# Performance work log

Hardware: AMD Instinct MI355X
Metric: run time of the kernel (lower is better)

## Reference

```python
import jax, jax.numpy as jnp
import numpy as np

THRESH1 = 0.8      # snn.Leaky threshold
THRESH2 = 1.0      # snn.Synaptic default threshold
FS_SLOPE = 25.0    # surrogate.fast_sigmoid default slope
ATAN_ALPHA = 2.0   # surrogate.atan default alpha
TIME_STEPS = 20

# --- surrogate-gradient spike fns (forward = Heaviside) ---
@jax.custom_vjp
def spike_fs(x):
    return (x > 0).astype(x.dtype)
def _fs_fwd(x):
    return (x > 0).astype(x.dtype), x
def _fs_bwd(res, g):
    return (g / (FS_SLOPE * jnp.abs(res) + 1.0) ** 2,)
spike_fs.defvjp(_fs_fwd, _fs_bwd)

@jax.custom_vjp
def spike_atan(x):
    return (x > 0).astype(x.dtype)
def _at_fwd(x):
    return (x > 0).astype(x.dtype), x
def _at_bwd(res, g):
    return (g * (ATAN_ALPHA / 2.0) / (1.0 + (jnp.pi / 2.0 * ATAN_ALPHA * res) ** 2),)
spike_atan.defvjp(_at_fwd, _at_bwd)


def setup_inputs() -> dict:
    key = jax.random.key(0)
    ks = jax.random.split(key, 4)
    V, E, H, B, S = 32000, 256, 512, 8, 16
    x = jax.random.randint(ks[0], (B, S), 0, V)
    embed = jax.random.normal(ks[1], (V, E), jnp.float32)
    W1 = jax.random.normal(ks[2], (H, E), jnp.float32) / jnp.sqrt(jnp.float32(E))
    b1 = jnp.zeros((H,), jnp.float32)
    W2 = jax.random.normal(ks[3], (V, H), jnp.float32) / jnp.sqrt(jnp.float32(H))
    b2 = jnp.zeros((V,), jnp.float32)
    return dict(x=x, embed=embed, W1=W1, b1=b1, W2=W2, b2=b2,
                beta1=jnp.float32(0.85), alpha2=jnp.float32(0.9), beta2=jnp.float32(0.8))


def _forward(x, embed, W1, b1, W2, b2, beta1, alpha2, beta2):
    B, S = x.shape
    V, H = W2.shape
    b1c = jnp.clip(beta1, 0.0, 1.0)   # snntorch clamps learnable decays
    a2c = jnp.clip(alpha2, 0.0, 1.0)
    b2c = jnp.clip(beta2, 0.0, 1.0)
    # cur1 = fc1(embed(x[:, t])) is constant within the inner time loop
    cur1_all = jnp.einsum('bse,he->bsh', embed[x], W1) + b1  # (B, S, H)

    def seq_step(carry, cur1_t):              # cur1_t: (B, H)
        mem1, syn2, mem2 = carry

        def time_step(c, _):
            mem1, syn2, mem2, _ = c
            # Leaky: reset (subtract) from PREVIOUS mem, detached
            reset1 = jax.lax.stop_gradient((mem1 - THRESH1 > 0).astype(mem1.dtype))
            mem1 = b1c * mem1 + cur1_t - reset1 * THRESH1
            spk1 = spike_fs(mem1 - THRESH1)
            cur2 = spk1 @ W2.T + b2            # (B, V)
            # Synaptic: syn = a*syn + cur; mem = b*mem + syn - reset*thr
            reset2 = jax.lax.stop_gradient((mem2 - THRESH2 > 0).astype(mem2.dtype))
            syn2 = a2c * syn2 + cur2
            mem2 = b2c * mem2 + syn2 - reset2 * THRESH2
            spk2 = spike_atan(mem2 - THRESH2)
            return (mem1, syn2, mem2, spk2), None

        spk2_init = jnp.zeros_like(mem2)
        (mem1, syn2, mem2, spk2), _ = jax.lax.scan(
            time_step, (mem1, syn2, mem2, spk2_init), None, length=TIME_STEPS)
        return (mem1, syn2, mem2), spk2       # only last inner spk2 is emitted

    mem1 = jnp.zeros((B, H), jnp.float32)
    syn2 = jnp.zeros((B, V), jnp.float32)
    mem2 = jnp.zeros((B, V), jnp.float32)
    (mem1, syn2, mem2), outs = jax.lax.scan(
        seq_step, (mem1, syn2, mem2), jnp.swapaxes(cur1_all, 0, 1))
    return jnp.swapaxes(outs, 0, 1), mem1, syn2, mem2   # (B, S, V), states


def reference(x, embed, W1, b1, W2, b2, beta1, alpha2, beta2):
    return _forward(x, embed, W1, b1, W2, b2, beta1, alpha2, beta2)
```

## Files before the change

### kernel.cpp

```cpp
#include <hip/hip_runtime.h>
#include <cstdint>

constexpr int NV = 32000;
constexpr int NE = 256;
constexpr int NH = 512;
constexpr int NB = 8;
constexpr int NS = 16;
constexpr int NT = 20;
constexpr float TH1 = 0.8f;
constexpr float TH2 = 1.0f;

typedef _Float16 f16x8 __attribute__((ext_vector_type(8)));
typedef float f32x4 __attribute__((ext_vector_type(4)));

__device__ inline float clip01(float v) { return fminf(fmaxf(v, 0.f), 1.f); }

#define GL_LDS(gp, lp) \
  __builtin_amdgcn_global_load_lds((const __attribute__((address_space(1))) void*)(gp), \
                                   (__attribute__((address_space(3))) void*)(lp), 16, 0, 0)

__device__ inline void barsched() {
  __builtin_amdgcn_s_barrier();
  __builtin_amdgcn_sched_barrier(0);
}

__global__ __launch_bounds__(64) void k_front(
    const int* __restrict__ x, const float* __restrict__ embed,
    const float* __restrict__ W1, const float* __restrict__ b1,
    const float* __restrict__ pbeta1,
    _Float16* __restrict__ A2P, float* __restrict__ mem1_out) {
  __shared__ float emb[16][256];
  const int tid = threadIdx.x;
  const int b   = blockIdx.x >> 3;
  const int hg  = blockIdx.x & 7;
  const int h   = hg * 64 + tid;

  for (int i = tid; i < 16 * 256; i += 64) {
    const int s = i >> 8;
    const int e = i & 255;
    emb[s][e] = embed[(size_t)x[b * 16 + s] * NE + e];
  }
  __syncthreads();

  float c[16];
#pragma unroll
  for (int s = 0; s < 16; ++s) c[s] = 0.f;
  const float* w = W1 + (size_t)h * NE;
  for (int e4 = 0; e4 < 64; ++e4) {
    const float4 wv = *(const float4*)(w + e4 * 4);
#pragma unroll
    for (int s = 0; s < 16; ++s) {
      const float4 ev = *(const float4*)&emb[s][e4 * 4];
      c[s] = fmaf(wv.w, ev.w, fmaf(wv.z, ev.z, fmaf(wv.y, ev.y, fmaf(wv.x, ev.x, c[s]))));
    }
  }
  const float bias = b1[h];
#pragma unroll
  for (int s = 0; s < 16; ++s) c[s] = c[s] + bias;

  const float bc = clip01(pbeta1[0]);
  const _Float16 one  = (_Float16)1.0f;
  const _Float16 zero = (_Float16)0.0f;
  const int ks  = hg;
  const int col = tid ^ (b << 3);
  float mem = 0.f;
  for (int s = 0; s < NS; ++s) {
    const float cs = c[s];
    for (int t = 0; t < NT; ++t) {
      float rst = (mem > TH1) ? TH1 : 0.f;
      mem = __fsub_rn(__fadd_rn(__fmul_rn(bc, mem), cs), rst);
      bool spk = mem > TH1;
      int gs = s * NT + t;
      size_t addr = ((size_t)((gs >> 3) * 8 + ks)) * 4096 + ((gs & 7) * 8 + b) * 64 + col;
      A2P[addr] = spk ? one : zero;
    }
  }
  mem1_out[b * NH + h] = mem;
}

__global__ __launch_bounds__(1024, 4) void k_fused(
    const _Float16* __restrict__ A2P,
    const float* __restrict__ W2,
    const float* __restrict__ b2,
    const float* __restrict__ pa2, const float* __restrict__ pb2,
    float* __restrict__ out) {
  __shared__ __attribute__((aligned(16))) _Float16 As[2 * 32768];

  const int tid  = threadIdx.x;
  const int lane = tid & 63;
  const int wid  = tid >> 6;
  const int kh   = wid >> 3;
  const int wm   = (wid >> 2) & 1;
  const int wn   = wid & 3;
  const int n0   = blockIdx.x * 128;

  const int lr  = lane & 15;
  const int lk8 = (lane >> 4) * 8;
  const int sw  = (lr & 7) * 8;
  const int cr  = (lane >> 4) * 4, cc = lane & 15;

  f16x8 bfr[2][8];
#pragma unroll
  for (int ni = 0; ni < 2; ++ni) {
    const int n = n0 + wn * 32 + ni * 16 + lr;
    const float* wp = W2 + (size_t)n * NH;
#pragma unroll
    for (int p = 0; p < 4; ++p) {
#pragma unroll
      for (int kf = 0; kf < 2; ++kf) {
        const int k0 = (kh * 4 + p) * 64 + kf * 32 + lk8;
        const float4 wa = *(const float4*)(wp + k0);
        const float4 wb = *(const float4*)(wp + k0 + 4);
        f16x8 v;
        v[0] = (_Float16)wa.x; v[1] = (_Float16)wa.y;
        v[2] = (_Float16)wa.z; v[3] = (_Float16)wa.w;
        v[4] = (_Float16)wb.x; v[5] = (_Float16)wb.y;
        v[6] = (_Float16)wb.z; v[7] = (_Float16)wb.w;
        bfr[ni][p * 2 + kf] = v;
      }
    }
  }

  const float a2  = clip01(pa2[0]);
  const float bcl = clip01(pb2[0]);
  const int vv = tid & 127;
  const int bb = tid >> 7;
  const float b2v = b2[n0 + vv];
  float syn = 0.f, mem = 0.f;
  unsigned spkmask = 0;
  f32x4 acc[2][2] = {};

  const _Float16* pA = A2P + wid * 512 + lane * 8;
  _Float16* dA = As + wid * 512;
  auto stage = [&](int g) {
    const _Float16* s = pA + (size_t)g * 32768;
    _Float16* d = dA + (g & 1) * 32768;
    GL_LDS(s,         d);
    GL_LDS(s + 8192,  d + 8192);
    GL_LDS(s + 16384, d + 16384);
    GL_LDS(s + 24576, d + 24576);
  };

  asm volatile("s_waitcnt vmcnt(0)" ::: "memory");
  barsched();
  stage(0);

#define CHUNK(C)                                                                 \
  {                                                                              \
    const int tb = sb + (kh * 4 + (C)) * 4096;                                   \
    {                                                                            \
      const int col = lk8 ^ sw;                                                  \
      const f16x8 a0 = *(const f16x8*)&As[tb + (wm * 32 + lr) * 64 + col];       \
      const f16x8 a1 = *(const f16x8*)&As[tb + (wm * 32 + 16 + lr) * 64 + col];  \
      acc[0][0] = __builtin_amdgcn_mfma_f32_16x16x32_f16(a0, bfr[0][(C)*2], acc[0][0], 0, 0, 0); \
      acc[1][0] = __builtin_amdgcn_mfma_f32_16x16x32_f16(a1, bfr[0][(C)*2], acc[1][0], 0, 0, 0); \
      acc[0][1] = __builtin_amdgcn_mfma_f32_16x16x32_f16(a0, bfr[1][(C)*2], acc[0][1], 0, 0, 0); \
      acc[1][1] = __builtin_amdgcn_mfma_f32_16x16x32_f16(a1, bfr[1][(C)*2], acc[1][1], 0, 0, 0); \
    }                                                                            \
    {                                                                            \
      const int col = (32 + lk8) ^ sw;                                           \
      const f16x8 a0 = *(const f16x8*)&As[tb + (wm * 32 + lr) * 64 + col];       \
      const f16x8 a1 = *(const f16x8*)&As[tb + (wm * 32 + 16 + lr) * 64 + col];  \
      acc[0][0] = __builtin_amdgcn_mfma_f32_16x16x32_f16(a0, bfr[0][(C)*2+1], acc[0][0], 0, 0, 0); \
      acc[1][0] = __builtin_amdgcn_mfma_f32_16x16x32_f16(a1, bfr[0][(C)*2+1], acc[1][0], 0, 0, 0); \
      acc[0][1] = __builtin_amdgcn_mfma_f32_16x16x32_f16(a0, bfr[1][(C)*2+1], acc[0][1], 0, 0, 0); \
      acc[1][1] = __builtin_amdgcn_mfma_f32_16x16x32_f16(a1, bfr[1][(C)*2+1], acc[1][1], 0, 0, 0); \
    }                                                                            \
  }

  for (int mt = 0; mt < 40; ++mt) {
    asm volatile("s_waitcnt vmcnt(0)" ::: "memory");
    barsched();
    if (mt < 39) stage(mt + 1);
    const int sb = (mt & 1) * 32768;
    CHUNK(0) CHUNK(1) CHUNK(2) CHUNK(3)
    barsched();
    float* Cl = (float*)&As[sb];
#pragma unroll
    for (int mi = 0; mi < 2; ++mi)
#pragma unroll
      for (int ni = 0; ni < 2; ++ni) {
#pragma unroll
        for (int j = 0; j < 4; ++j)
          Cl[((wm * 32 + mi * 16 + cr + j) * 128 + wn * 32 + ni * 16 + cc) * 2 + kh] = acc[mi][ni][j];
        acc[mi][ni] = (f32x4){0.f, 0.f, 0.f, 0.f};
      }
    barsched();
#pragma unroll
    for (int st = 0; st < 8; ++st) {
      const int gs = mt * 8 + st;
      const float2 c2 = *(const float2*)&Cl[((st * 8 + bb) * 128 + vv) * 2];
      float cur2 = __fadd_rn(__fadd_rn(c2.x, c2.y), b2v);
      float rst = (mem > TH2) ? 1.f : 0.f;
      syn = __fadd_rn(__fmul_rn(a2, syn), cur2);
      mem = __fsub_rn(__fadd_rn(__fmul_rn(bcl, mem), syn), rst);
      if (gs % 20 == 19)
        spkmask |= (mem > TH2 ? 1u : 0u) << (gs / 20);
    }
  }
#undef CHUNK

#pragma unroll
  for (int s = 0; s < NS; ++s)
    out[((size_t)bb * NS + s) * NV + n0 + vv] = (spkmask >> s) & 1 ? 1.f : 0.f;
  out[(size_t)4100096 + (size_t)bb * NV + n0 + vv] = syn;
  out[(size_t)4356096 + (size_t)bb * NV + n0 + vv] = mem;
}

extern "C" void kernel_launch(void* const* d_in, const int* in_sizes, int n_in,
                              void* d_out, int out_size, void* d_ws, size_t ws_size,
                              hipStream_t stream) {
  const int*   x     = (const int*)d_in[0];
  const float* embed = (const float*)d_in[1];
  const float* W1    = (const float*)d_in[2];
  const float* b1    = (const float*)d_in[3];
  const float* W2    = (const float*)d_in[4];
  const float* b2    = (const float*)d_in[5];
  const float* pb1   = (const float*)d_in[6];
  const float* pa2   = (const float*)d_in[7];
  const float* pb2   = (const float*)d_in[8];
  float* out = (float*)d_out;

  _Float16* A2P = (_Float16*)d_ws;

  hipLaunchKernelGGL(k_front, dim3(64), dim3(64), 0, stream,
                     x, embed, W1, b1, pb1, A2P, out + 4096000);
  hipLaunchKernelGGL(k_fused, dim3(NV / 128), dim3(1024), 0, stream,
                     A2P, W2, b2, pa2, pb2, out);
}
```

Before: 144.8 us.

## Merge front and fused kernels into one cooperative kernel with grid sync

Merges the embedding/fc1/Leaky front kernel into the main MFMA kernel, launched cooperatively over 250 blocks. The first 16 blocks compute the spike matrix while every block loads its W2 fragments, and a grid-wide sync separates the two phases. This removes one kernel launch and lets the W2 register loads overlap with the front computation. In exchange, the front work now reads embedding rows straight from global memory instead of LDS and runs on only 256 threads per block, and the grid sync adds a barrier cost; the cooperative launch also requires all 250 blocks to be co-resident.

```diff
diff --git a/kernel.cpp b/kernel.cpp
--- a/kernel.cpp
+++ b/kernel.cpp
@@ -1,5 +1,8 @@
 #include <hip/hip_runtime.h>
+#include <hip/hip_cooperative_groups.h>
 #include <cstdint>
+
+namespace cg = cooperative_groups;
 
 constexpr int NV = 32000;
 constexpr int NE = 256;
@@ -24,66 +27,13 @@
   __builtin_amdgcn_sched_barrier(0);
 }
 
-__global__ __launch_bounds__(64) void k_front(
+__global__ __launch_bounds__(1024, 4) void k_all(
     const int* __restrict__ x, const float* __restrict__ embed,
     const float* __restrict__ W1, const float* __restrict__ b1,
-    const float* __restrict__ pbeta1,
-    _Float16* __restrict__ A2P, float* __restrict__ mem1_out) {
-  __shared__ float emb[16][256];
-  const int tid = threadIdx.x;
-  const int b   = blockIdx.x >> 3;
-  const int hg  = blockIdx.x & 7;
-  const int h   = hg * 64 + tid;
-
-  for (int i = tid; i < 16 * 256; i += 64) {
-    const int s = i >> 8;
-    const int e = i & 255;
-    emb[s][e] = embed[(size_t)x[b * 16 + s] * NE + e];
-  }
-  __syncthreads();
-
-  float c[16];
-#pragma unroll
-  for (int s = 0; s < 16; ++s) c[s] = 0.f;
-  const float* w = W1 + (size_t)h * NE;
-  for (int e4 = 0; e4 < 64; ++e4) {
-    const float4 wv = *(const float4*)(w + e4 * 4);
-#pragma unroll
-    for (int s = 0; s < 16; ++s) {
-      const float4 ev = *(const float4*)&emb[s][e4 * 4];
-      c[s] = fmaf(wv.w, ev.w, fmaf(wv.z, ev.z, fmaf(wv.y, ev.y, fmaf(wv.x, ev.x, c[s]))));
-    }
-  }
-  const float bias = b1[h];
-#pragma unroll
-  for (int s = 0; s < 16; ++s) c[s] = c[s] + bias;
-
-  const float bc = clip01(pbeta1[0]);
-  const _Float16 one  = (_Float16)1.0f;
-  const _Float16 zero = (_Float16)0.0f;
-  const int ks  = hg;
-  const int col = tid ^ (b << 3);
-  float mem = 0.f;
-  for (int s = 0; s < NS; ++s) {
-    const float cs = c[s];
-    for (int t = 0; t < NT; ++t) {
-      float rst = (mem > TH1) ? TH1 : 0.f;
-      mem = __fsub_rn(__fadd_rn(__fmul_rn(bc, mem), cs), rst);
-      bool spk = mem > TH1;
-      int gs = s * NT + t;
-      size_t addr = ((size_t)((gs >> 3) * 8 + ks)) * 4096 + ((gs & 7) * 8 + b) * 64 + col;
-      A2P[addr] = spk ? one : zero;
-    }
-  }
-  mem1_out[b * NH + h] = mem;
-}
-
-__global__ __launch_bounds__(1024, 4) void k_fused(
-    const _Float16* __restrict__ A2P,
-    const float* __restrict__ W2,
-    const float* __restrict__ b2,
+    const float* __restrict__ pb1,
+    const float* __restrict__ W2, const float* __restrict__ b2,
     const float* __restrict__ pa2, const float* __restrict__ pb2,
-    float* __restrict__ out) {
+    _Float16* __restrict__ A2P, float* __restrict__ out) {
   __shared__ __attribute__((aligned(16))) _Float16 As[2 * 32768];
 
   const int tid  = threadIdx.x;
@@ -98,6 +48,49 @@
   const int lk8 = (lane >> 4) * 8;
   const int sw  = (lr & 7) * 8;
   const int cr  = (lane >> 4) * 4, cc = lane & 15;
+
+  if (blockIdx.x < 16 && tid < 256) {
+    const int g = blockIdx.x * 256 + tid;
+    const int b = g >> 9, h = g & 511;
+    int xrow[16];
+#pragma unroll
+    for (int s = 0; s < 16; ++s) xrow[s] = x[b * 16 + s];
+
+    float c[16];
+#pragma unroll
+    for (int s = 0; s < 16; ++s) c[s] = 0.f;
+    const float* w = W1 + (size_t)h * NE;
+    for (int e4 = 0; e4 < 64; ++e4) {
+      const float4 wv = *(const float4*)(w + e4 * 4);
+#pragma unroll
+      for (int s = 0; s < 16; ++s) {
+        const float4 ev = *(const float4*)&embed[(size_t)xrow[s] * NE + e4 * 4];
+        c[s] = fmaf(wv.w, ev.w, fmaf(wv.z, ev.z, fmaf(wv.y, ev.y, fmaf(wv.x, ev.x, c[s]))));
+      }
+    }
+    const float bias = b1[h];
+#pragma unroll
+    for (int s = 0; s < 16; ++s) c[s] = c[s] + bias;
+
+    const float bc = clip01(pb1[0]);
+    const _Float16 one  = (_Float16)1.0f;
+    const _Float16 zero = (_Float16)0.0f;
+    const int ks  = h >> 6;
+    const int col = (h & 63) ^ (b << 3);
+    float mem = 0.f;
+    for (int s = 0; s < NS; ++s) {
+      const float cs = c[s];
+      for (int t = 0; t < NT; ++t) {
+        float rst = (mem > TH1) ? TH1 : 0.f;
+        mem = __fsub_rn(__fadd_rn(__fmul_rn(bc, mem), cs), rst);
+        bool spk = mem > TH1;
+        int gs = s * NT + t;
+        size_t addr = ((size_t)((gs >> 3) * 8 + ks)) * 4096 + ((gs & 7) * 8 + b) * 64 + col;
+        A2P[addr] = spk ? one : zero;
+      }
+    }
+    out[(size_t)4096000 + b * NH + h] = mem;
+  }
 
   f16x8 bfr[2][8];
 #pragma unroll
@@ -120,6 +113,8 @@
       }
     }
   }
+
+  cg::this_grid().sync();
 
   const float a2  = clip01(pa2[0]);
   const float bcl = clip01(pb2[0]);
@@ -223,8 +218,9 @@
 
   _Float16* A2P = (_Float16*)d_ws;
 
-  hipLaunchKernelGGL(k_front, dim3(64), dim3(64), 0, stream,
-                     x, embed, W1, b1, pb1, A2P, out + 4096000);
-  hipLaunchKernelGGL(k_fused, dim3(NV / 128), dim3(1024), 0, stream,
-                     A2P, W2, b2, pa2, pb2, out);
+  void* args[] = {(void*)&x, (void*)&embed, (void*)&W1, (void*)&b1, (void*)&pb1,
+                  (void*)&W2, (void*)&b2, (void*)&pa2, (void*)&pb2,
+                  (void*)&A2P, (void*)&out};
+  hipLaunchCooperativeKernel((const void*)k_all, dim3(NV / 128), dim3(1024),
+                             args, 0, stream);
 }
```

Result: slower. 210.6 us (+45.5%).
